# Kernel optimization log

Hardware: AMD Instinct MI355X
Metric: run time of the kernel (lower is better)

The kernel has to match this reference:

```python
import jax, jax.numpy as jnp
import numpy as np

B, DIM_IN, T = 16, 512, 2048
DIM_OUT2 = 512 * 2  # dim_out * 2 (GLU halves it)
K = 3
STYLE = 128
SCALE_CONV = 1.0 / np.sqrt(DIM_IN * K ** 2).astype(np.float32)  # fan_in = dim_in * k^2 (as in source)
SCALE_LIN = 1.0 / np.sqrt(STYLE).astype(np.float32)


def setup_inputs() -> dict:
    key = jax.random.key(0)
    ks = jax.random.split(key, 6)
    x = jax.random.normal(ks[0], (B, DIM_IN, T), dtype=jnp.float32)
    c_src = jax.random.normal(ks[1], (B, STYLE), dtype=jnp.float32)
    c_trg = jax.random.normal(ks[2], (B, STYLE), dtype=jnp.float32)
    # EqualLinear params (lr_mul=1): weight ~ N(0,1), bias filled with bias_init=1
    w_s = jax.random.normal(ks[3], (DIM_IN, STYLE), dtype=jnp.float32)
    b_s = jnp.ones((DIM_IN,), dtype=jnp.float32)
    w_b = jax.random.normal(ks[4], (DIM_IN, STYLE), dtype=jnp.float32)
    b_b = jnp.ones((DIM_IN,), dtype=jnp.float32)
    weight = jax.random.normal(ks[5], (1, DIM_OUT2, DIM_IN, K), dtype=jnp.float32)
    return {"x": x, "c_src": c_src, "c_trg": c_trg,
            "w_s": w_s, "b_s": b_s, "w_b": w_b, "b_b": b_b, "weight": weight}


def reference(x, c_src, c_trg, w_s, b_s, w_b, b_b, weight):
    bsz, cin, t = x.shape
    cout = weight.shape[1]  # dim_out * 2
    k = weight.shape[3]
    # EqualLinear: F.linear(c, w*scale, bias)
    s = (c_trg @ (w_s * SCALE_LIN).T + b_s).reshape(bsz, 1, cin, 1)
    beta = (c_trg @ (w_b * SCALE_LIN).T + b_b).reshape(bsz, 1, cin, 1)
    w = SCALE_CONV * (weight * s + beta)               # [B, Cout, Cin, K]
    demod = jax.lax.rsqrt(jnp.sum(w * w, axis=(2, 3)) + 1e-8)   # [B, Cout]
    demod_mean = jnp.mean(w.reshape(bsz, cout, -1), axis=2)      # [B, Cout]
    w = (w - demod_mean[:, :, None, None]) * demod[:, :, None, None]
    # batch-as-groups conv1d
    w = w.reshape(bsz * cout, cin, k)
    xr = x.reshape(1, bsz * cin, t)
    out = jax.lax.conv_general_dilated(
        xr, w, window_strides=(1,), padding=[(k // 2, k // 2)],
        dimension_numbers=("NCH", "OIH", "NCH"), feature_group_count=bsz)
    out = out.reshape(bsz, cout, -1)
    a, g = jnp.split(out, 2, axis=1)  # GLU on channel dim
    return a * jax.nn.sigmoid(g)
```

## Files before the change

kernel.cpp:

```cpp
#include <hip/hip_runtime.h>
#include <math.h>

typedef __attribute__((ext_vector_type(8))) short short8;
typedef __attribute__((ext_vector_type(16))) float f32x16;
typedef unsigned short ushortT;

#define NB     16
#define CIN    512
#define TT     2048
#define COUT2  1024
#define NSTYLE 128
#define KKTOT  1536
#define TPAD   2050
#define NKT    24

#define SCALE_LIN  0.088388347648318447f
#define SCALE_CONV 0.014731391274719736f

__device__ __forceinline__ ushortT f2bf(float f) {
  union { float f; unsigned u; } v; v.f = f;
  unsigned r = v.u + 0x7fffu + ((v.u >> 16) & 1u);
  return (ushortT)(r >> 16);
}

__device__ __forceinline__ void gload16(const void* g, void* l) {
  __builtin_amdgcn_global_load_lds(
      (const __attribute__((address_space(1))) void*)g,
      (__attribute__((address_space(3))) void*)l, 16, 0, 0);
}

__global__ void style_kernel(const float* __restrict__ c_trg,
                             const float* __restrict__ w_s, const float* __restrict__ b_s,
                             const float* __restrict__ w_b, const float* __restrict__ b_b,
                             float* __restrict__ s, float* __restrict__ beta,
                             ushortT* __restrict__ xT) {
  int gid = blockIdx.x * 256 + threadIdx.x;
  int b = gid >> 9, ci = gid & 511;
  const float* ct = c_trg + b * NSTYLE;
  const float* ws = w_s + ci * NSTYLE;
  const float* wb = w_b + ci * NSTYLE;
  float as = 0.f, ab = 0.f;
#pragma unroll 8
  for (int j = 0; j < NSTYLE; ++j) {
    float c = ct[j];
    as += c * ws[j];
    ab += c * wb[j];
  }
  s[gid]    = as * SCALE_LIN + b_s[ci];
  beta[gid] = ab * SCALE_LIN + b_b[ci];
  xT[(size_t)b * TPAD * CIN + ci] = 0;
  xT[((size_t)b * TPAD + TPAD - 1) * CIN + ci] = 0;
}

__global__ void xpose_kernel(const float* __restrict__ x, ushortT* __restrict__ xT) {
  int b = blockIdx.z, ct = blockIdx.y, tt = blockIdx.x;
  int t0 = tt * 64, ci0 = ct * 64;
  __shared__ float tile[64][65];
  const float* xB = x + (size_t)b * CIN * TT;
  int rr = threadIdx.x >> 4;
  int c4 = threadIdx.x & 15;
#pragma unroll
  for (int it = 0; it < 4; ++it) {
    int ci = rr + it * 16;
    float4 v = *(const float4*)(xB + (size_t)(ci0 + ci) * TT + t0 + c4 * 4);
    tile[ci][c4 * 4 + 0] = v.x; tile[ci][c4 * 4 + 1] = v.y;
    tile[ci][c4 * 4 + 2] = v.z; tile[ci][c4 * 4 + 3] = v.w;
  }
  __syncthreads();
  ushortT* xTB = xT + (size_t)b * TPAD * CIN;
#pragma unroll
  for (int it = 0; it < 4; ++it) {
    int t = rr + it * 16;
    ushort4 o;
    o.x = f2bf(tile[c4 * 4 + 0][t]); o.y = f2bf(tile[c4 * 4 + 1][t]);
    o.z = f2bf(tile[c4 * 4 + 2][t]); o.w = f2bf(tile[c4 * 4 + 3][t]);
    *(ushort4*)(xTB + (size_t)(1 + t0 + t) * CIN + ci0 + c4 * 4) = o;
  }
}

__global__ void modw_kernel(const float* __restrict__ weight,
                            const float* __restrict__ s, const float* __restrict__ beta,
                            ushortT* __restrict__ wnorm) {
  int co = blockIdx.x, b = blockIdx.y, tid = threadIdx.x;
  int ci = tid * 2;
  const float* wp = weight + (size_t)co * CIN * 3 + (size_t)ci * 3;
  float s0 = s[b * CIN + ci],     s1 = s[b * CIN + ci + 1];
  float e0 = beta[b * CIN + ci],  e1 = beta[b * CIN + ci + 1];
  float w0 = SCALE_CONV * (wp[0] * s0 + e0);
  float w1 = SCALE_CONV * (wp[1] * s0 + e0);
  float w2 = SCALE_CONV * (wp[2] * s0 + e0);
  float w3 = SCALE_CONV * (wp[3] * s1 + e1);
  float w4 = SCALE_CONV * (wp[4] * s1 + e1);
  float w5 = SCALE_CONV * (wp[5] * s1 + e1);
  float sum = w0 + w1 + w2 + w3 + w4 + w5;
  float sq  = w0*w0 + w1*w1 + w2*w2 + w3*w3 + w4*w4 + w5*w5;
#pragma unroll
  for (int off = 32; off; off >>= 1) {
    sum += __shfl_xor(sum, off);
    sq  += __shfl_xor(sq,  off);
  }
  __shared__ float rs[4], rq[4];
  if ((tid & 63) == 0) { rs[tid >> 6] = sum; rq[tid >> 6] = sq; }
  __syncthreads();
  float tsum = rs[0] + rs[1] + rs[2] + rs[3];
  float tsq  = rq[0] + rq[1] + rq[2] + rq[3];
  float mean  = tsum * (1.0f / 1536.0f);
  float demod = rsqrtf(tsq + 1e-8f);
  int r = ((co & 511) << 1) | (co >> 9);
  ushortT* dst = wnorm + ((size_t)b * COUT2 + r) * KKTOT;
  ushort2 p0, p1, p2;
  p0.x = f2bf((w0 - mean) * demod); p0.y = f2bf((w3 - mean) * demod);
  p1.x = f2bf((w1 - mean) * demod); p1.y = f2bf((w4 - mean) * demod);
  p2.x = f2bf((w2 - mean) * demod); p2.y = f2bf((w5 - mean) * demod);
  *(ushort2*)(dst +        ci) = p0;
  *(ushort2*)(dst +  512 + ci) = p1;
  *(ushort2*)(dst + 1024 + ci) = p2;
}


#define AF(d, s, m, k) (*(const short8*)(ldsc + ((d) * 4 + (s)) * 16384 + arow + (m) * 2048 + ((k) ? colk1 : colk0)))
#define BF(d, s, n, k) (*(const short8*)(ldsc + ((d) * 4 + 2 + (s)) * 16384 + brow + (n) * 2048 + ((k) ? colk1 : colk0)))

#define STAGE_A(d, s, kt) do { int kc_ = (kt) * 64 + (s) * 32;                  \
    gload16(sA0 + kc_, ldsw + ((d) * 4 + (s)) * 8192 + dst8);                   \
    gload16(sA1 + kc_, ldsw + ((d) * 4 + (s)) * 8192 + 4096 + dst8);            \
  } while (0)

#define STAGE_B(d, s, kt) do { int kc_ = (kt) * 64 + (s) * 32;                  \
    gload16(sB0 + kc_, ldsw + ((d) * 4 + 2 + (s)) * 8192 + dst8);               \
    gload16(sB1 + kc_, ldsw + ((d) * 4 + 2 + (s)) * 8192 + 4096 + dst8);        \
  } while (0)

#define PHASE(d, s, STAGES, VMN) do {                                           \
    short8 af[4][2], bfr[2][2];                                                 \
    _Pragma("unroll") for (int m_ = 0; m_ < 4; ++m_) {                          \
      af[m_][0] = AF(d, s, m_, 0); af[m_][1] = AF(d, s, m_, 1);                 \
    }                                                                           \
    _Pragma("unroll") for (int n_ = 0; n_ < 2; ++n_) {                          \
      bfr[n_][0] = BF(d, s, n_, 0); bfr[n_][1] = BF(d, s, n_, 1);               \
    }                                                                           \
    STAGES;                                                                     \
    if ((VMN) == 8)      asm volatile("s_waitcnt vmcnt(8)" ::: "memory");       \
    else if ((VMN) == 4) asm volatile("s_waitcnt vmcnt(4)" ::: "memory");       \
    else if ((VMN) == 0) asm volatile("s_waitcnt vmcnt(0)" ::: "memory");       \
    __builtin_amdgcn_sched_barrier(0);                                          \
    __builtin_amdgcn_s_barrier();                                               \
    __builtin_amdgcn_sched_barrier(0);                                          \
    __builtin_amdgcn_s_setprio(1);                                              \
    _Pragma("unroll") for (int k_ = 0; k_ < 2; ++k_)                            \
      _Pragma("unroll") for (int m_ = 0; m_ < 4; ++m_)                          \
        _Pragma("unroll") for (int n_ = 0; n_ < 2; ++n_)                        \
          acc[m_][n_] = __builtin_amdgcn_mfma_f32_32x32x16_bf16(                \
              af[m_][k_], bfr[n_][k_], acc[m_][n_], 0, 0, 0);                   \
    __builtin_amdgcn_s_setprio(0);                                              \
    __builtin_amdgcn_sched_barrier(0);                                          \
    __builtin_amdgcn_s_barrier();                                               \
    __builtin_amdgcn_sched_barrier(0);                                          \
  } while (0)

__global__ __launch_bounds__(512, 2)
void conv_gemm8(const ushortT* __restrict__ wnorm, const ushortT* __restrict__ xT,
                float* __restrict__ out) {
  extern __shared__ ushortT ldsw[];
  const char* ldsc = (const char*)ldsw;

  int orig = blockIdx.x;
  int wgid = (orig & 7) * 64 + (orig >> 3);
  int b  = wgid >> 5;
  int i5 = wgid & 31;
  int mp = i5 >> 4, r2 = i5 & 15;
  int nt = r2 >> 1, mt = mp * 2 + (r2 & 1);
  int co0 = mt * 256, t0 = nt * 256;

  int tid = threadIdx.x;
  int l = tid & 63, w = tid >> 6;
  int wm = w & 1, wn = w >> 1;

  int r0 = tid >> 2;
  int jbs8 = (((tid & 3) ^ ((r0 >> 1) & 3)) << 3);
  int dst8 = tid * 8;
  int sw = (l >> 1) & 3;
  int arow = (wm * 128 + (l & 31)) * 64;
  int brow = (wn * 64  + (l & 31)) * 64;
  int colk0 = (((l >> 5)    ) ^ sw) * 16;
  int colk1 = (((l >> 5) | 2) ^ sw) * 16;

  const ushortT* wB = wnorm + (size_t)b * COUT2 * KKTOT;
  const ushortT* xB = xT + (size_t)b * TPAD * CIN;
  const ushortT* sA0 = wB + (size_t)(co0 + r0) * KKTOT + jbs8;
  const ushortT* sA1 = sA0 + (size_t)128 * KKTOT;
  const ushortT* sB0 = xB + (size_t)(t0 + r0) * CIN + jbs8;
  const ushortT* sB1 = sB0 + (size_t)128 * CIN;

  f32x16 acc[4][2] = {};

  STAGE_A(0, 0, 0); STAGE_B(0, 0, 0);
  STAGE_A(0, 1, 0); STAGE_B(0, 1, 0);
  STAGE_A(1, 0, 1); STAGE_B(1, 0, 1);
  asm volatile("s_waitcnt vmcnt(8)" ::: "memory");
  __builtin_amdgcn_sched_barrier(0);
  __builtin_amdgcn_s_barrier();
  __builtin_amdgcn_sched_barrier(0);

  for (int j = 0; j < 11; ++j) {
    int kt1 = 2 * j + 1;
    int k0n = 2 * j + 2, k1n = 2 * j + 3;
    PHASE(0, 0, { STAGE_A(1, 1, kt1); STAGE_B(1, 1, kt1); }, 8);
    PHASE(0, 1, { STAGE_A(0, 0, k0n); STAGE_B(0, 0, k0n); }, 8);
    PHASE(1, 0, { STAGE_A(0, 1, k0n); STAGE_B(0, 1, k0n); }, 8);
    PHASE(1, 1, { STAGE_A(1, 0, k1n); STAGE_B(1, 0, k1n); }, 8);
  }
  PHASE(0, 0, { STAGE_A(1, 1, 23); STAGE_B(1, 1, 23); }, 8);
  PHASE(0, 1, {}, 4);
  PHASE(1, 0, {}, 0);
  PHASE(1, 1, {}, -1);

  int hi4 = (l >> 5) * 4;
#pragma unroll
  for (int m = 0; m < 4; ++m) {
    int cobase = co0 + wm * 128 + m * 32;
#pragma unroll
    for (int n = 0; n < 2; ++n) {
      int t = t0 + wn * 64 + n * 32 + (l & 31);
      f32x16 v = acc[m][n];
#pragma unroll
      for (int q = 0; q < 8; ++q) {
        int row = 2 * (q & 1) + 8 * (q >> 1) + hi4;
        int c = (cobase + row) >> 1;
        float a = v[2 * q], g = v[2 * q + 1];
        out[((size_t)b * (COUT2 / 2) + c) * TT + t] = a / (1.f + __expf(-g));
      }
    }
  }
}

extern "C" void kernel_launch(void* const* d_in, const int* in_sizes, int n_in,
                              void* d_out, int out_size, void* d_ws, size_t ws_size,
                              hipStream_t stream) {
  const float* x      = (const float*)d_in[0];
  const float* c_trg  = (const float*)d_in[2];
  const float* w_s    = (const float*)d_in[3];
  const float* b_s    = (const float*)d_in[4];
  const float* w_b    = (const float*)d_in[5];
  const float* b_b    = (const float*)d_in[6];
  const float* weight = (const float*)d_in[7];
  float* out = (float*)d_out;

  char* ws = (char*)d_ws;
  float*   s     = (float*)ws;
  float*   beta  = (float*)(ws + 32768);
  ushortT* xT    = (ushortT*)(ws + 65536);
  ushortT* wnorm = (ushortT*)(ws + 65536 + 33587200);

  hipFuncSetAttribute((const void*)conv_gemm8,
                      hipFuncAttributeMaxDynamicSharedMemorySize, 131072);

  style_kernel<<<32, 256, 0, stream>>>(c_trg, w_s, b_s, w_b, b_b, s, beta, xT);
  xpose_kernel<<<dim3(32, 8, 16), 256, 0, stream>>>(x, xT);
  modw_kernel<<<dim3(1024, 16), 256, 0, stream>>>(weight, s, beta, wnorm);
  conv_gemm8<<<512, 512, 131072, stream>>>(wnorm, xT, out);
}
```

Measured before the change: 148.8 us.

## Rework conv GEMM to 256x128 tiles with 16x16 MFMA and loop modw over batch

```diff
diff --git a/kernel.cpp b/kernel.cpp
--- a/kernel.cpp
+++ b/kernel.cpp
@@ -2,7 +2,7 @@
 #include <math.h>
 
 typedef __attribute__((ext_vector_type(8))) short short8;
-typedef __attribute__((ext_vector_type(16))) float f32x16;
+typedef __attribute__((ext_vector_type(4))) float f32x4;
 typedef unsigned short ushortT;
 
 #define NB     16
@@ -12,7 +12,7 @@
 #define NSTYLE 128
 #define KKTOT  1536
 #define TPAD   2050
-#define NKT    24
+#define NT32   48
 
 #define SCALE_LIN  0.088388347648318447f
 #define SCALE_CONV 0.014731391274719736f
@@ -81,155 +81,149 @@
 __global__ void modw_kernel(const float* __restrict__ weight,
                             const float* __restrict__ s, const float* __restrict__ beta,
                             ushortT* __restrict__ wnorm) {
-  int co = blockIdx.x, b = blockIdx.y, tid = threadIdx.x;
+  int co = blockIdx.x, tid = threadIdx.x;
   int ci = tid * 2;
-  const float* wp = weight + (size_t)co * CIN * 3 + (size_t)ci * 3;
-  float s0 = s[b * CIN + ci],     s1 = s[b * CIN + ci + 1];
-  float e0 = beta[b * CIN + ci],  e1 = beta[b * CIN + ci + 1];
-  float w0 = SCALE_CONV * (wp[0] * s0 + e0);
-  float w1 = SCALE_CONV * (wp[1] * s0 + e0);
-  float w2 = SCALE_CONV * (wp[2] * s0 + e0);
-  float w3 = SCALE_CONV * (wp[3] * s1 + e1);
-  float w4 = SCALE_CONV * (wp[4] * s1 + e1);
-  float w5 = SCALE_CONV * (wp[5] * s1 + e1);
-  float sum = w0 + w1 + w2 + w3 + w4 + w5;
-  float sq  = w0*w0 + w1*w1 + w2*w2 + w3*w3 + w4*w4 + w5*w5;
-#pragma unroll
-  for (int off = 32; off; off >>= 1) {
-    sum += __shfl_xor(sum, off);
-    sq  += __shfl_xor(sq,  off);
-  }
+  const float* wp = weight + (size_t)co * KKTOT + (size_t)ci * 3;
+  float2 va = *(const float2*)(wp);
+  float2 vb = *(const float2*)(wp + 2);
+  float2 vc = *(const float2*)(wp + 4);
+  float v0 = va.x, v1 = va.y, v2 = vb.x, v3 = vb.y, v4 = vc.x, v5 = vc.y;
+  int r = ((co & 511) << 1) | (co >> 9);
   __shared__ float rs[4], rq[4];
-  if ((tid & 63) == 0) { rs[tid >> 6] = sum; rq[tid >> 6] = sq; }
-  __syncthreads();
-  float tsum = rs[0] + rs[1] + rs[2] + rs[3];
-  float tsq  = rq[0] + rq[1] + rq[2] + rq[3];
-  float mean  = tsum * (1.0f / 1536.0f);
-  float demod = rsqrtf(tsq + 1e-8f);
-  int r = ((co & 511) << 1) | (co >> 9);
-  ushortT* dst = wnorm + ((size_t)b * COUT2 + r) * KKTOT;
-  ushort2 p0, p1, p2;
-  p0.x = f2bf((w0 - mean) * demod); p0.y = f2bf((w3 - mean) * demod);
-  p1.x = f2bf((w1 - mean) * demod); p1.y = f2bf((w4 - mean) * demod);
-  p2.x = f2bf((w2 - mean) * demod); p2.y = f2bf((w5 - mean) * demod);
-  *(ushort2*)(dst +        ci) = p0;
-  *(ushort2*)(dst +  512 + ci) = p1;
-  *(ushort2*)(dst + 1024 + ci) = p2;
-}
-
-
-#define AF(d, s, m, k) (*(const short8*)(ldsc + ((d) * 4 + (s)) * 16384 + arow + (m) * 2048 + ((k) ? colk1 : colk0)))
-#define BF(d, s, n, k) (*(const short8*)(ldsc + ((d) * 4 + 2 + (s)) * 16384 + brow + (n) * 2048 + ((k) ? colk1 : colk0)))
-
-#define STAGE_A(d, s, kt) do { int kc_ = (kt) * 64 + (s) * 32;                  \
-    gload16(sA0 + kc_, ldsw + ((d) * 4 + (s)) * 8192 + dst8);                   \
-    gload16(sA1 + kc_, ldsw + ((d) * 4 + (s)) * 8192 + 4096 + dst8);            \
+  for (int b = 0; b < NB; ++b) {
+    float2 sv = *(const float2*)(s + b * CIN + ci);
+    float2 ev = *(const float2*)(beta + b * CIN + ci);
+    float w0 = SCALE_CONV * (v0 * sv.x + ev.x);
+    float w1 = SCALE_CONV * (v1 * sv.x + ev.x);
+    float w2 = SCALE_CONV * (v2 * sv.x + ev.x);
+    float w3 = SCALE_CONV * (v3 * sv.y + ev.y);
+    float w4 = SCALE_CONV * (v4 * sv.y + ev.y);
+    float w5 = SCALE_CONV * (v5 * sv.y + ev.y);
+    float sum = w0 + w1 + w2 + w3 + w4 + w5;
+    float sq  = w0*w0 + w1*w1 + w2*w2 + w3*w3 + w4*w4 + w5*w5;
+#pragma unroll
+    for (int off = 32; off; off >>= 1) {
+      sum += __shfl_xor(sum, off);
+      sq  += __shfl_xor(sq,  off);
+    }
+    if ((tid & 63) == 0) { rs[tid >> 6] = sum; rq[tid >> 6] = sq; }
+    __syncthreads();
+    float mean  = (rs[0] + rs[1] + rs[2] + rs[3]) * (1.0f / 1536.0f);
+    float demod = rsqrtf(rq[0] + rq[1] + rq[2] + rq[3] + 1e-8f);
+    ushortT* dst = wnorm + ((size_t)b * COUT2 + r) * KKTOT;
+    ushort2 p0, p1, p2;
+    p0.x = f2bf((w0 - mean) * demod); p0.y = f2bf((w3 - mean) * demod);
+    p1.x = f2bf((w1 - mean) * demod); p1.y = f2bf((w4 - mean) * demod);
+    p2.x = f2bf((w2 - mean) * demod); p2.y = f2bf((w5 - mean) * demod);
+    *(ushort2*)(dst +        ci) = p0;
+    *(ushort2*)(dst +  512 + ci) = p1;
+    *(ushort2*)(dst + 1024 + ci) = p2;
+    __syncthreads();
+  }
+}
+
+
+#define AFRAG(d, f) (*(const short8*)(ldsc + (d) * 24576 + aoff + (f) * 1024))
+#define BFRAG(d, g) (*(const short8*)(ldsc + (d) * 24576 + 16384 + boff + (g) * 1024))
+
+#define STAGE(dn, kt) do { int kc_ = (kt) * 32;                                 \
+    gload16(sA0 + kc_, ldsw + (dn) * 12288 + dst8);                             \
+    gload16(sA1 + kc_, ldsw + (dn) * 12288 + 4096 + dst8);                      \
+    gload16(sB0 + kc_, ldsw + (dn) * 12288 + 8192 + dst8);                      \
   } while (0)
 
-#define STAGE_B(d, s, kt) do { int kc_ = (kt) * 64 + (s) * 32;                  \
-    gload16(sB0 + kc_, ldsw + ((d) * 4 + 2 + (s)) * 8192 + dst8);               \
-    gload16(sB1 + kc_, ldsw + ((d) * 4 + 2 + (s)) * 8192 + 4096 + dst8);        \
-  } while (0)
-
-#define PHASE(d, s, STAGES, VMN) do {                                           \
-    short8 af[4][2], bfr[2][2];                                                 \
-    _Pragma("unroll") for (int m_ = 0; m_ < 4; ++m_) {                          \
-      af[m_][0] = AF(d, s, m_, 0); af[m_][1] = AF(d, s, m_, 1);                 \
-    }                                                                           \
-    _Pragma("unroll") for (int n_ = 0; n_ < 2; ++n_) {                          \
-      bfr[n_][0] = BF(d, s, n_, 0); bfr[n_][1] = BF(d, s, n_, 1);               \
-    }                                                                           \
-    STAGES;                                                                     \
-    if ((VMN) == 8)      asm volatile("s_waitcnt vmcnt(8)" ::: "memory");       \
-    else if ((VMN) == 4) asm volatile("s_waitcnt vmcnt(4)" ::: "memory");       \
-    else if ((VMN) == 0) asm volatile("s_waitcnt vmcnt(0)" ::: "memory");       \
+#define TILE(dc, ktn, DO_STAGE) do {                                            \
+    short8 af0 = AFRAG(dc, 0), af1 = AFRAG(dc, 1);                              \
+    short8 af2 = AFRAG(dc, 2), af3 = AFRAG(dc, 3);                              \
+    short8 bf0 = BFRAG(dc, 0), bf1 = BFRAG(dc, 1);                              \
+    short8 bf2 = BFRAG(dc, 2), bf3 = BFRAG(dc, 3);                              \
+    if (DO_STAGE) STAGE((dc) ^ 1, ktn);                                         \
+    __builtin_amdgcn_s_setprio(1);                                              \
+    acc[0][0] = __builtin_amdgcn_mfma_f32_16x16x32_bf16(af0, bf0, acc[0][0], 0, 0, 0); \
+    acc[0][1] = __builtin_amdgcn_mfma_f32_16x16x32_bf16(af0, bf1, acc[0][1], 0, 0, 0); \
+    acc[0][2] = __builtin_amdgcn_mfma_f32_16x16x32_bf16(af0, bf2, acc[0][2], 0, 0, 0); \
+    acc[0][3] = __builtin_amdgcn_mfma_f32_16x16x32_bf16(af0, bf3, acc[0][3], 0, 0, 0); \
+    acc[1][0] = __builtin_amdgcn_mfma_f32_16x16x32_bf16(af1, bf0, acc[1][0], 0, 0, 0); \
+    acc[1][1] = __builtin_amdgcn_mfma_f32_16x16x32_bf16(af1, bf1, acc[1][1], 0, 0, 0); \
+    acc[1][2] = __builtin_amdgcn_mfma_f32_16x16x32_bf16(af1, bf2, acc[1][2], 0, 0, 0); \
+    acc[1][3] = __builtin_amdgcn_mfma_f32_16x16x32_bf16(af1, bf3, acc[1][3], 0, 0, 0); \
+    acc[2][0] = __builtin_amdgcn_mfma_f32_16x16x32_bf16(af2, bf0, acc[2][0], 0, 0, 0); \
+    acc[2][1] = __builtin_amdgcn_mfma_f32_16x16x32_bf16(af2, bf1, acc[2][1], 0, 0, 0); \
+    acc[2][2] = __builtin_amdgcn_mfma_f32_16x16x32_bf16(af2, bf2, acc[2][2], 0, 0, 0); \
+    acc[2][3] = __builtin_amdgcn_mfma_f32_16x16x32_bf16(af2, bf3, acc[2][3], 0, 0, 0); \
+    acc[3][0] = __builtin_amdgcn_mfma_f32_16x16x32_bf16(af3, bf0, acc[3][0], 0, 0, 0); \
+    acc[3][1] = __builtin_amdgcn_mfma_f32_16x16x32_bf16(af3, bf1, acc[3][1], 0, 0, 0); \
+    acc[3][2] = __builtin_amdgcn_mfma_f32_16x16x32_bf16(af3, bf2, acc[3][2], 0, 0, 0); \
+    acc[3][3] = __builtin_amdgcn_mfma_f32_16x16x32_bf16(af3, bf3, acc[3][3], 0, 0, 0); \
+    __builtin_amdgcn_s_setprio(0);                                              \
     __builtin_amdgcn_sched_barrier(0);                                          \
-    __builtin_amdgcn_s_barrier();                                               \
-    __builtin_amdgcn_sched_barrier(0);                                          \
-    __builtin_amdgcn_s_setprio(1);                                              \
-    _Pragma("unroll") for (int k_ = 0; k_ < 2; ++k_)                            \
-      _Pragma("unroll") for (int m_ = 0; m_ < 4; ++m_)                          \
-        _Pragma("unroll") for (int n_ = 0; n_ < 2; ++n_)                        \
-          acc[m_][n_] = __builtin_amdgcn_mfma_f32_32x32x16_bf16(                \
-              af[m_][k_], bfr[n_][k_], acc[m_][n_], 0, 0, 0);                   \
-    __builtin_amdgcn_s_setprio(0);                                              \
+    asm volatile("s_waitcnt vmcnt(0)" ::: "memory");                            \
     __builtin_amdgcn_sched_barrier(0);                                          \
     __builtin_amdgcn_s_barrier();                                               \
     __builtin_amdgcn_sched_barrier(0);                                          \
   } while (0)
 
-__global__ __launch_bounds__(512, 2)
-void conv_gemm8(const ushortT* __restrict__ wnorm, const ushortT* __restrict__ xT,
-                float* __restrict__ out) {
+__global__ __launch_bounds__(512, 4)
+void conv_gemm(const ushortT* __restrict__ wnorm, const ushortT* __restrict__ xT,
+               float* __restrict__ out) {
   extern __shared__ ushortT ldsw[];
   const char* ldsc = (const char*)ldsw;
 
   int orig = blockIdx.x;
-  int wgid = (orig & 7) * 64 + (orig >> 3);
-  int b  = wgid >> 5;
-  int i5 = wgid & 31;
-  int mp = i5 >> 4, r2 = i5 & 15;
-  int nt = r2 >> 1, mt = mp * 2 + (r2 & 1);
-  int co0 = mt * 256, t0 = nt * 256;
+  int wgid = (orig & 7) * 128 + (orig >> 3);
+  int b  = wgid >> 6;
+  int mt = (wgid >> 4) & 3;
+  int nt = wgid & 15;
+  int co0 = mt * 256, t0 = nt * 128;
 
   int tid = threadIdx.x;
   int l = tid & 63, w = tid >> 6;
-  int wm = w & 1, wn = w >> 1;
+  int wm = w >> 1, wn = w & 1;
 
   int r0 = tid >> 2;
   int jbs8 = (((tid & 3) ^ ((r0 >> 1) & 3)) << 3);
   int dst8 = tid * 8;
-  int sw = (l >> 1) & 3;
-  int arow = (wm * 128 + (l & 31)) * 64;
-  int brow = (wn * 64  + (l & 31)) * 64;
-  int colk0 = (((l >> 5)    ) ^ sw) * 16;
-  int colk1 = (((l >> 5) | 2) ^ sw) * 16;
+  int cb = ((l >> 4) ^ ((l >> 1) & 3));
+  int aoff = (wm * 64 + (l & 15)) * 64 + cb * 16;
+  int boff = (wn * 64 + (l & 15)) * 64 + cb * 16;
 
   const ushortT* wB = wnorm + (size_t)b * COUT2 * KKTOT;
   const ushortT* xB = xT + (size_t)b * TPAD * CIN;
   const ushortT* sA0 = wB + (size_t)(co0 + r0) * KKTOT + jbs8;
   const ushortT* sA1 = sA0 + (size_t)128 * KKTOT;
   const ushortT* sB0 = xB + (size_t)(t0 + r0) * CIN + jbs8;
-  const ushortT* sB1 = sB0 + (size_t)128 * CIN;
-
-  f32x16 acc[4][2] = {};
-
-  STAGE_A(0, 0, 0); STAGE_B(0, 0, 0);
-  STAGE_A(0, 1, 0); STAGE_B(0, 1, 0);
-  STAGE_A(1, 0, 1); STAGE_B(1, 0, 1);
-  asm volatile("s_waitcnt vmcnt(8)" ::: "memory");
+
+  f32x4 acc[4][4];
+#pragma unroll
+  for (int i = 0; i < 4; ++i)
+#pragma unroll
+    for (int j = 0; j < 4; ++j)
+      acc[i][j] = (f32x4){0.f, 0.f, 0.f, 0.f};
+
+  STAGE(0, 0);
+  asm volatile("s_waitcnt vmcnt(0)" ::: "memory");
   __builtin_amdgcn_sched_barrier(0);
   __builtin_amdgcn_s_barrier();
   __builtin_amdgcn_sched_barrier(0);
 
-  for (int j = 0; j < 11; ++j) {
-    int kt1 = 2 * j + 1;
-    int k0n = 2 * j + 2, k1n = 2 * j + 3;
-    PHASE(0, 0, { STAGE_A(1, 1, kt1); STAGE_B(1, 1, kt1); }, 8);
-    PHASE(0, 1, { STAGE_A(0, 0, k0n); STAGE_B(0, 0, k0n); }, 8);
-    PHASE(1, 0, { STAGE_A(0, 1, k0n); STAGE_B(0, 1, k0n); }, 8);
-    PHASE(1, 1, { STAGE_A(1, 0, k1n); STAGE_B(1, 0, k1n); }, 8);
-  }
-  PHASE(0, 0, { STAGE_A(1, 1, 23); STAGE_B(1, 1, 23); }, 8);
-  PHASE(0, 1, {}, 4);
-  PHASE(1, 0, {}, 0);
-  PHASE(1, 1, {}, -1);
-
-  int hi4 = (l >> 5) * 4;
-#pragma unroll
-  for (int m = 0; m < 4; ++m) {
-    int cobase = co0 + wm * 128 + m * 32;
-#pragma unroll
-    for (int n = 0; n < 2; ++n) {
-      int t = t0 + wn * 64 + n * 32 + (l & 31);
-      f32x16 v = acc[m][n];
-#pragma unroll
-      for (int q = 0; q < 8; ++q) {
-        int row = 2 * (q & 1) + 8 * (q >> 1) + hi4;
-        int c = (cobase + row) >> 1;
-        float a = v[2 * q], g = v[2 * q + 1];
-        out[((size_t)b * (COUT2 / 2) + c) * TT + t] = a / (1.f + __expf(-g));
-      }
+  for (int j = 0; j < 23; ++j) {
+    TILE(0, 2 * j + 1, 1);
+    TILE(1, 2 * j + 2, 1);
+  }
+  TILE(0, 47, 1);
+  TILE(1, 0, 0);
+
+#pragma unroll
+  for (int mi = 0; mi < 4; ++mi) {
+    int cop = co0 + wm * 64 + mi * 16 + ((l >> 4) << 2);
+    int c = cop >> 1;
+    size_t obase = ((size_t)b * (COUT2 / 2) + c) * TT;
+#pragma unroll
+    for (int ni = 0; ni < 4; ++ni) {
+      int t = t0 + wn * 64 + ni * 16 + (l & 15);
+      f32x4 v = acc[mi][ni];
+      out[obase + t]      = v.x / (1.f + __expf(-v.y));
+      out[obase + TT + t] = v.z / (1.f + __expf(-v.w));
     }
   }
 }
@@ -252,11 +246,11 @@
   ushortT* xT    = (ushortT*)(ws + 65536);
   ushortT* wnorm = (ushortT*)(ws + 65536 + 33587200);
 
-  hipFuncSetAttribute((const void*)conv_gemm8,
-                      hipFuncAttributeMaxDynamicSharedMemorySize, 131072);
+  hipFuncSetAttribute((const void*)conv_gemm,
+                      hipFuncAttributeMaxDynamicSharedMemorySize, 49152);
 
   style_kernel<<<32, 256, 0, stream>>>(c_trg, w_s, b_s, w_b, b_b, s, beta, xT);
   xpose_kernel<<<dim3(32, 8, 16), 256, 0, stream>>>(x, xT);
-  modw_kernel<<<dim3(1024, 16), 256, 0, stream>>>(weight, s, beta, wnorm);
-  conv_gemm8<<<512, 512, 131072, stream>>>(wnorm, xT, out);
-}
+  modw_kernel<<<1024, 256, 0, stream>>>(weight, s, beta, wnorm);
+  conv_gemm<<<1024, 512, 49152, stream>>>(wnorm, xT, out);
+}
```

New measurement: 151.7 us. About the same (+1.9%).
